# Optimization experiments

Measured on AMD Instinct MI355X. Metric: run time of the kernel, lower is better.

Reference implementation:

```python
import jax, jax.numpy as jnp
import numpy as np
from jax import lax

VOCAB, EMB, HID, B, T = 512, 128, 64, 256, 1024

def setup_inputs() -> dict:
    key = jax.random.key(0)
    ks = jax.random.split(key, 16)
    s = 0.1  # small init to keep tanh in its linear-ish range
    return {
        'x': jax.random.randint(ks[0], (B, T), 0, VOCAB),
        'emb': jax.random.normal(ks[1], (VOCAB, EMB), jnp.float32) * s,
        'Wih0': jax.random.normal(ks[2], (HID, EMB), jnp.float32) * s,
        'Whh0': jax.random.normal(ks[3], (HID, HID), jnp.float32) * s,
        'bih0': jax.random.normal(ks[4], (HID,), jnp.float32) * s,
        'bhh0': jax.random.normal(ks[5], (HID,), jnp.float32) * s,
        'Wih1': jax.random.normal(ks[6], (HID, HID), jnp.float32) * s,
        'Whh1': jax.random.normal(ks[7], (HID, HID), jnp.float32) * s,
        'bih1': jax.random.normal(ks[8], (HID,), jnp.float32) * s,
        'bhh1': jax.random.normal(ks[9], (HID,), jnp.float32) * s,
        'W1': jax.random.normal(ks[10], (32, HID), jnp.float32) * s,
        'b1': jax.random.normal(ks[11], (32,), jnp.float32) * s,
        'W2': jax.random.normal(ks[12], (1, 32), jnp.float32) * s,
        'b2': jax.random.normal(ks[13], (1,), jnp.float32) * s,
    }

def _rnn_layer(xs, Wih, Whh, bih, bhh):
    # xs: [T, B, D_in]; PyTorch cell: h_t = tanh(x W_ih^T + b_ih + h W_hh^T + b_hh)
    bsz = xs.shape[1]
    h0 = jnp.zeros((bsz, Whh.shape[0]), xs.dtype)
    def step(h, xt):
        h = jnp.tanh(xt @ Wih.T + bih + h @ Whh.T + bhh)
        return h, h
    hN, out = lax.scan(step, h0, xs)
    return hN, out

def reference(x, emb, Wih0, Whh0, bih0, bhh0, Wih1, Whh1, bih1, bhh1, W1, b1, W2, b2):
    xe = emb[x]                      # [B, T, EMB] embedding gather
    xs = jnp.swapaxes(xe, 0, 1)      # [T, B, EMB] time-major for scan
    _, out1 = _rnn_layer(xs, Wih0, Whh0, bih0, bhh0)   # layer 0 (dropout=0 in eval)
    hN, _ = _rnn_layer(out1, Wih1, Whh1, bih1, bhh1)   # layer 1; hN == h_n[-1]
    y = jnp.maximum(hN @ W1.T + b1, 0.0) @ W2.T + b2   # [B, 1]
    return y
```

## Files before the change

kernel.cpp:

```cpp
#include <hip/hip_runtime.h>

#define VOCAB 512
#define EMB   128
#define HID   64
#define BATCH 256
#define TLEN  1024
#define CH    8
#define NCH   (TLEN / CH)
#define RS    64
#define RCH   (RS / CH)
#define RW    80

typedef float v2f __attribute__((ext_vector_type(2)));

__device__ __forceinline__ float fast_tanh(float x) {
    float e = __expf(2.0f * x);
    return 1.0f - 2.0f / (e + 1.0f);
}
__device__ __forceinline__ void lds_fence() {
    asm volatile("s_waitcnt lgkmcnt(0)" ::: "memory");
}
__device__ __forceinline__ void compiler_fence() {
    asm volatile("" ::: "memory");
}
__device__ __forceinline__ void nap() { __builtin_amdgcn_s_sleep(1); }

__device__ __forceinline__ float quad_sum(float x) {
    int t1 = __builtin_amdgcn_update_dpp(0, __float_as_int(x), 0xB1, 0xF, 0xF, false);
    float s = x + __int_as_float(t1);
    int t2 = __builtin_amdgcn_update_dpp(0, __float_as_int(s), 0x4E, 0xF, 0xF, false);
    return s + __int_as_float(t2);
}

__device__ __forceinline__ float dot_seg(const float4 s[4], const v2f w[4][8],
                                         int kg) {
    float z0, z1, z2, z3;
    #pragma unroll
    for (int r = 0; r < 4; ++r) {
        v2f a0 = v2f{0.f, 0.f}, a1 = v2f{0.f, 0.f};
        #pragma unroll
        for (int c = 0; c < 4; ++c) {
            float4 u = s[c];
            a0 = __builtin_elementwise_fma(v2f{u.x, u.y}, w[r][2 * c],     a0);
            a1 = __builtin_elementwise_fma(v2f{u.z, u.w}, w[r][2 * c + 1], a1);
        }
        float zr = quad_sum((a0.x + a0.y) + (a1.x + a1.y));
        if (r == 0) z0 = zr; else if (r == 1) z1 = zr;
        else if (r == 2) z2 = zr; else z3 = zr;
    }
    return (kg & 1) ? ((kg & 2) ? z3 : z1) : ((kg & 2) ? z2 : z0);
}

__device__ __forceinline__ void load_w(v2f w[4][8], const float* __restrict__ W,
                                       int o, int kg) {
    #pragma unroll
    for (int r = 0; r < 4; ++r) {
        const float4* wr = (const float4*)(W + (o + 16 * r) * HID + 16 * kg);
        #pragma unroll
        for (int c = 0; c < 4; ++c) {
            float4 u = wr[c];
            w[r][2 * c]     = v2f{u.x, u.y};
            w[r][2 * c + 1] = v2f{u.z, u.w};
        }
    }
}

__device__ __forceinline__ void seg_load(float4 s[4], const float* rowkg) {
    const float4* p = (const float4*)rowkg;
    #pragma unroll
    for (int c = 0; c < 4; ++c) s[c] = p[c];
}

__global__ void __launch_bounds__(64) p0_kernel(
    const float* __restrict__ emb,
    const float* __restrict__ wih0,
    const float* __restrict__ bih0,
    const float* __restrict__ bhh0,
    float* __restrict__ P0)
{
    const int v = blockIdx.x;
    const int i = threadIdx.x;
    const float4* er = (const float4*)(emb  + v * EMB);
    const float4* wr = (const float4*)(wih0 + i * EMB);
    float a0 = 0.f, a1 = 0.f, a2 = 0.f, a3 = 0.f;
    #pragma unroll
    for (int k = 0; k < EMB / 4; ++k) {
        float4 e4 = er[k];
        float4 w4 = wr[k];
        a0 = fmaf(e4.x, w4.x, a0);
        a1 = fmaf(e4.y, w4.y, a1);
        a2 = fmaf(e4.z, w4.z, a2);
        a3 = fmaf(e4.w, w4.w, a3);
    }
    P0[v * HID + i] = (a0 + a1) + (a2 + a3) + bih0[i] + bhh0[i];
}

__global__ void __launch_bounds__(192, 1) rnn_kernel(
    const int*   __restrict__ xs,
    const float* __restrict__ P0,
    const float* __restrict__ Whh0,
    const float* __restrict__ Wih1,
    const float* __restrict__ Whh1,
    const float* __restrict__ bih1,
    const float* __restrict__ bhh1,
    const float* __restrict__ W1,
    const float* __restrict__ b1,
    const float* __restrict__ W2,
    const float* __restrict__ b2,
    float*       __restrict__ out)
{
    __shared__ float h0ring[RS][RW];
    __shared__ float p1ring[RS][HID];
    __shared__ float h1buf[2][RW];
    __shared__ int   flags[3];

    const int b    = blockIdx.x;
    const int tid  = threadIdx.x;
    const int wv   = tid >> 6;
    const int lane = tid & 63;
    const int o    = lane >> 2;
    const int kg   = lane & 3;
    const int row  = o + 16 * kg;
    const int wrs  = 20 * kg + o;

    const int* xrow = xs + b * TLEN;
    const int vz = (int)__builtin_amdgcn_mbcnt_lo(0u, 0u);

    if (tid < 3) flags[tid] = 0;
    __syncthreads();

    volatile int* vf = (volatile int*)flags;

    if (wv == 0) {
        v2f w0[4][8];
        load_w(w0, Whh0, o, kg);

        int   xv_old[CH];
        float a_old[CH];
        #pragma unroll
        for (int i = 0; i < CH; ++i)
            xv_old[i] = xrow[CH + i + vz] & (VOCAB - 1);
        #pragma unroll
        for (int i = 0; i < CH; ++i)
            a_old[i] = P0[(xrow[i + vz] & (VOCAB - 1)) * HID + row];

        float4 s0[4];
        #pragma unroll
        for (int c = 0; c < 4; ++c) s0[c] = float4{0.f, 0.f, 0.f, 0.f};

        #pragma unroll 1
        for (int k = 0; k < NCH; ++k) {
            if (k >= RCH) {
                while (vf[1] < k - (RCH - 1)) nap();
                compiler_fence();
            }
            const int  c2  = (k + 2 < NCH) ? (k + 2) : (NCH - 1);
            const int* xp  = xrow + c2 * CH;
            int   xv_new[CH];
            float a_new[CH];
            #pragma unroll
            for (int i = 0; i < CH; ++i)
                xv_new[i] = xp[i + vz] & (VOCAB - 1);
            #pragma unroll
            for (int i = 0; i < CH; ++i)
                a_new[i] = P0[xv_old[i] * HID + row];

            const int base = (k & (RCH - 1)) * CH;
            #pragma unroll
            for (int i = 0; i < CH; ++i) {
                float z  = dot_seg(s0, w0, kg) + a_old[i];
                float hv = fast_tanh(z);
                h0ring[base + i][wrs] = hv;
                seg_load(s0, &h0ring[base + i][20 * kg]);
            }
            lds_fence();
            if (lane == 0) vf[0] = k + 1;

            #pragma unroll
            for (int i = 0; i < CH; ++i) { a_old[i] = a_new[i]; xv_old[i] = xv_new[i]; }
        }
    } else if (wv == 1) {
        v2f wp[4][8];
        load_w(wp, Wih1, o, kg);
        const float b1s = bih1[row] + bhh1[row];

        #pragma unroll 1
        for (int k = 0; k < NCH; ++k) {
            while (vf[0] < k + 1) nap();
            if (k >= RCH) { while (vf[2] < k - (RCH - 1)) nap(); }
            compiler_fence();
            const int base = (k & (RCH - 1)) * CH;
            float4 c0[4];
            seg_load(c0, &h0ring[base][20 * kg]);
            #pragma unroll
            for (int i = 0; i < CH; ++i) {
                float4 nx[4];
                if (i < CH - 1) seg_load(nx, &h0ring[base + i + 1][20 * kg]);
                float pv = dot_seg(c0, wp, kg) + b1s;
                p1ring[base + i][row] = pv;
                if (i < CH - 1) {
                    #pragma unroll
                    for (int c = 0; c < 4; ++c) c0[c] = nx[c];
                }
            }
            lds_fence();
            if (lane == 0) vf[1] = k + 1;
        }
    } else {
        v2f w2[4][8];
        load_w(w2, Whh1, o, kg);

        float4 s1[4];
        #pragma unroll
        for (int c = 0; c < 4; ++c) s1[c] = float4{0.f, 0.f, 0.f, 0.f};

        #pragma unroll 1
        for (int k = 0; k < NCH; ++k) {
            while (vf[1] < k + 1) nap();
            compiler_fence();
            const int base = (k & (RCH - 1)) * CH;
            float p[CH];
            #pragma unroll
            for (int i = 0; i < CH; ++i) p[i] = p1ring[base + i][row];
            #pragma unroll
            for (int i = 0; i < CH; ++i) {
                const int t = k * CH + i;
                float z  = dot_seg(s1, w2, kg) + p[i];
                float hv = fast_tanh(z);
                h1buf[t & 1][wrs] = hv;
                seg_load(s1, &h1buf[t & 1][20 * kg]);
            }
            lds_fence();
            if (lane == 0) vf[2] = k + 1;
        }
        float r = 0.f;
        if (lane < 32) {
            float acc = b1[lane];
            const float* w1row = W1 + lane * HID;
            const float* hN    = h1buf[(TLEN - 1) & 1];
            #pragma unroll
            for (int j = 0; j < HID; ++j)
                acc = fmaf(w1row[j], hN[20 * (j >> 4) + (j & 15)], acc);
            r = fmaxf(acc, 0.f) * W2[lane];
        }
        #pragma unroll
        for (int off = 32; off > 0; off >>= 1) r += __shfl_down(r, off);
        if (lane == 0) out[b] = r + b2[0];
    }
}

extern "C" void kernel_launch(void* const* d_in, const int* in_sizes, int n_in,
                              void* d_out, int out_size, void* d_ws, size_t ws_size,
                              hipStream_t stream)
{
    const int*   x    = (const int*)d_in[0];
    const float* emb  = (const float*)d_in[1];
    const float* Wih0 = (const float*)d_in[2];
    const float* Whh0 = (const float*)d_in[3];
    const float* bih0 = (const float*)d_in[4];
    const float* bhh0 = (const float*)d_in[5];
    const float* Wih1 = (const float*)d_in[6];
    const float* Whh1 = (const float*)d_in[7];
    const float* bih1 = (const float*)d_in[8];
    const float* bhh1 = (const float*)d_in[9];
    const float* W1   = (const float*)d_in[10];
    const float* b1   = (const float*)d_in[11];
    const float* W2   = (const float*)d_in[12];
    const float* b2   = (const float*)d_in[13];

    float* P0 = (float*)d_ws;

    hipLaunchKernelGGL(p0_kernel, dim3(VOCAB), dim3(HID), 0, stream,
                       emb, Wih0, bih0, bhh0, P0);
    hipLaunchKernelGGL(rnn_kernel, dim3(BATCH), dim3(192), 0, stream,
                       x, P0, Whh0, Wih1, Whh1, bih1, bhh1,
                       W1, b1, W2, b2, (float*)d_out);
}
```

Baseline: 308.1 us.

## Process two batch rows per block to interleave independent recurrences

Each block now runs two batch sequences at once. Every wave interleaves the two independent recurrence chains (dot, tanh, LDS store and reload) so one chain's latency can hide behind the other's work. The grid is halved to 128 blocks, leaving half the CUs idle, and the LDS ring depth is halved so the doubled buffers still fit, which tightens the producer/consumer slack between waves.

```diff
diff --git a/kernel.cpp b/kernel.cpp
--- a/kernel.cpp
+++ b/kernel.cpp
@@ -7,7 +7,7 @@
 #define TLEN  1024
 #define CH    8
 #define NCH   (TLEN / CH)
-#define RS    64
+#define RS    32
 #define RCH   (RS / CH)
 #define RW    80
 
@@ -109,12 +109,13 @@
     const float* __restrict__ b2,
     float*       __restrict__ out)
 {
-    __shared__ float h0ring[RS][RW];
-    __shared__ float p1ring[RS][HID];
-    __shared__ float h1buf[2][RW];
+    __shared__ float h0ring[2][RS][RW];
+    __shared__ float p1ring[2][RS][HID];
+    __shared__ float h1buf[2][2][RW];
     __shared__ int   flags[3];
 
-    const int b    = blockIdx.x;
+    const int b0   = blockIdx.x * 2;
+    const int b1i  = b0 + 1;
     const int tid  = threadIdx.x;
     const int wv   = tid >> 6;
     const int lane = tid & 63;
@@ -123,7 +124,8 @@
     const int row  = o + 16 * kg;
     const int wrs  = 20 * kg + o;
 
-    const int* xrow = xs + b * TLEN;
+    const int* xr0 = xs + b0  * TLEN;
+    const int* xr1 = xs + b1i * TLEN;
     const int vz = (int)__builtin_amdgcn_mbcnt_lo(0u, 0u);
 
     if (tid < 3) flags[tid] = 0;
@@ -135,18 +137,25 @@
         v2f w0[4][8];
         load_w(w0, Whh0, o, kg);
 
-        int   xv_old[CH];
-        float a_old[CH];
-        #pragma unroll
-        for (int i = 0; i < CH; ++i)
-            xv_old[i] = xrow[CH + i + vz] & (VOCAB - 1);
-        #pragma unroll
-        for (int i = 0; i < CH; ++i)
-            a_old[i] = P0[(xrow[i + vz] & (VOCAB - 1)) * HID + row];
-
-        float4 s0[4];
-        #pragma unroll
-        for (int c = 0; c < 4; ++c) s0[c] = float4{0.f, 0.f, 0.f, 0.f};
+        int   xv_old[2][CH];
+        float a_old[2][CH];
+        #pragma unroll
+        for (int i = 0; i < CH; ++i) {
+            xv_old[0][i] = xr0[CH + i + vz] & (VOCAB - 1);
+            xv_old[1][i] = xr1[CH + i + vz] & (VOCAB - 1);
+        }
+        #pragma unroll
+        for (int i = 0; i < CH; ++i) {
+            a_old[0][i] = P0[(xr0[i + vz] & (VOCAB - 1)) * HID + row];
+            a_old[1][i] = P0[(xr1[i + vz] & (VOCAB - 1)) * HID + row];
+        }
+
+        float4 s0[4], s1[4];
+        #pragma unroll
+        for (int c = 0; c < 4; ++c) {
+            s0[c] = float4{0.f, 0.f, 0.f, 0.f};
+            s1[c] = float4{0.f, 0.f, 0.f, 0.f};
+        }
 
         #pragma unroll 1
         for (int k = 0; k < NCH; ++k) {
@@ -155,29 +164,41 @@
                 compiler_fence();
             }
             const int  c2  = (k + 2 < NCH) ? (k + 2) : (NCH - 1);
-            const int* xp  = xrow + c2 * CH;
-            int   xv_new[CH];
-            float a_new[CH];
-            #pragma unroll
-            for (int i = 0; i < CH; ++i)
-                xv_new[i] = xp[i + vz] & (VOCAB - 1);
-            #pragma unroll
-            for (int i = 0; i < CH; ++i)
-                a_new[i] = P0[xv_old[i] * HID + row];
+            const int* xp0 = xr0 + c2 * CH;
+            const int* xp1 = xr1 + c2 * CH;
+            int   xv_new[2][CH];
+            float a_new[2][CH];
+            #pragma unroll
+            for (int i = 0; i < CH; ++i) {
+                xv_new[0][i] = xp0[i + vz] & (VOCAB - 1);
+                xv_new[1][i] = xp1[i + vz] & (VOCAB - 1);
+            }
+            #pragma unroll
+            for (int i = 0; i < CH; ++i) {
+                a_new[0][i] = P0[xv_old[0][i] * HID + row];
+                a_new[1][i] = P0[xv_old[1][i] * HID + row];
+            }
 
             const int base = (k & (RCH - 1)) * CH;
             #pragma unroll
             for (int i = 0; i < CH; ++i) {
-                float z  = dot_seg(s0, w0, kg) + a_old[i];
-                float hv = fast_tanh(z);
-                h0ring[base + i][wrs] = hv;
-                seg_load(s0, &h0ring[base + i][20 * kg]);
+                float z0  = dot_seg(s0, w0, kg) + a_old[0][i];
+                float z1  = dot_seg(s1, w0, kg) + a_old[1][i];
+                float h0v = fast_tanh(z0);
+                float h1v = fast_tanh(z1);
+                h0ring[0][base + i][wrs] = h0v;
+                h0ring[1][base + i][wrs] = h1v;
+                seg_load(s0, &h0ring[0][base + i][20 * kg]);
+                seg_load(s1, &h0ring[1][base + i][20 * kg]);
             }
             lds_fence();
             if (lane == 0) vf[0] = k + 1;
 
             #pragma unroll
-            for (int i = 0; i < CH; ++i) { a_old[i] = a_new[i]; xv_old[i] = xv_new[i]; }
+            for (int i = 0; i < CH; ++i) {
+                a_old[0][i] = a_new[0][i]; xv_old[0][i] = xv_new[0][i];
+                a_old[1][i] = a_new[1][i]; xv_old[1][i] = xv_new[1][i];
+            }
         }
     } else if (wv == 1) {
         v2f wp[4][8];
@@ -190,17 +211,23 @@
             if (k >= RCH) { while (vf[2] < k - (RCH - 1)) nap(); }
             compiler_fence();
             const int base = (k & (RCH - 1)) * CH;
-            float4 c0[4];
-            seg_load(c0, &h0ring[base][20 * kg]);
-            #pragma unroll
-            for (int i = 0; i < CH; ++i) {
-                float4 nx[4];
-                if (i < CH - 1) seg_load(nx, &h0ring[base + i + 1][20 * kg]);
-                float pv = dot_seg(c0, wp, kg) + b1s;
-                p1ring[base + i][row] = pv;
+            float4 c0[4], c1[4];
+            seg_load(c0, &h0ring[0][base][20 * kg]);
+            seg_load(c1, &h0ring[1][base][20 * kg]);
+            #pragma unroll
+            for (int i = 0; i < CH; ++i) {
+                float4 n0[4], n1[4];
+                if (i < CH - 1) {
+                    seg_load(n0, &h0ring[0][base + i + 1][20 * kg]);
+                    seg_load(n1, &h0ring[1][base + i + 1][20 * kg]);
+                }
+                float pv0 = dot_seg(c0, wp, kg) + b1s;
+                float pv1 = dot_seg(c1, wp, kg) + b1s;
+                p1ring[0][base + i][row] = pv0;
+                p1ring[1][base + i][row] = pv1;
                 if (i < CH - 1) {
                     #pragma unroll
-                    for (int c = 0; c < 4; ++c) c0[c] = nx[c];
+                    for (int c = 0; c < 4; ++c) { c0[c] = n0[c]; c1[c] = n1[c]; }
                 }
             }
             lds_fence();
@@ -210,42 +237,55 @@
         v2f w2[4][8];
         load_w(w2, Whh1, o, kg);
 
-        float4 s1[4];
-        #pragma unroll
-        for (int c = 0; c < 4; ++c) s1[c] = float4{0.f, 0.f, 0.f, 0.f};
+        float4 s0[4], s1[4];
+        #pragma unroll
+        for (int c = 0; c < 4; ++c) {
+            s0[c] = float4{0.f, 0.f, 0.f, 0.f};
+            s1[c] = float4{0.f, 0.f, 0.f, 0.f};
+        }
 
         #pragma unroll 1
         for (int k = 0; k < NCH; ++k) {
             while (vf[1] < k + 1) nap();
             compiler_fence();
             const int base = (k & (RCH - 1)) * CH;
-            float p[CH];
-            #pragma unroll
-            for (int i = 0; i < CH; ++i) p[i] = p1ring[base + i][row];
+            float p0v[CH], p1v[CH];
+            #pragma unroll
+            for (int i = 0; i < CH; ++i) {
+                p0v[i] = p1ring[0][base + i][row];
+                p1v[i] = p1ring[1][base + i][row];
+            }
             #pragma unroll
             for (int i = 0; i < CH; ++i) {
                 const int t = k * CH + i;
-                float z  = dot_seg(s1, w2, kg) + p[i];
-                float hv = fast_tanh(z);
-                h1buf[t & 1][wrs] = hv;
-                seg_load(s1, &h1buf[t & 1][20 * kg]);
+                float z0  = dot_seg(s0, w2, kg) + p0v[i];
+                float z1  = dot_seg(s1, w2, kg) + p1v[i];
+                float h0v = fast_tanh(z0);
+                float h1v = fast_tanh(z1);
+                h1buf[0][t & 1][wrs] = h0v;
+                h1buf[1][t & 1][wrs] = h1v;
+                seg_load(s0, &h1buf[0][t & 1][20 * kg]);
+                seg_load(s1, &h1buf[1][t & 1][20 * kg]);
             }
             lds_fence();
             if (lane == 0) vf[2] = k + 1;
         }
-        float r = 0.f;
-        if (lane < 32) {
-            float acc = b1[lane];
-            const float* w1row = W1 + lane * HID;
-            const float* hN    = h1buf[(TLEN - 1) & 1];
-            #pragma unroll
-            for (int j = 0; j < HID; ++j)
-                acc = fmaf(w1row[j], hN[20 * (j >> 4) + (j & 15)], acc);
-            r = fmaxf(acc, 0.f) * W2[lane];
-        }
-        #pragma unroll
-        for (int off = 32; off > 0; off >>= 1) r += __shfl_down(r, off);
-        if (lane == 0) out[b] = r + b2[0];
+        #pragma unroll 1
+        for (int s = 0; s < 2; ++s) {
+            float r = 0.f;
+            if (lane < 32) {
+                float acc = b1[lane];
+                const float* w1row = W1 + lane * HID;
+                const float* hN    = h1buf[s][(TLEN - 1) & 1];
+                #pragma unroll
+                for (int j = 0; j < HID; ++j)
+                    acc = fmaf(w1row[j], hN[20 * (j >> 4) + (j & 15)], acc);
+                r = fmaxf(acc, 0.f) * W2[lane];
+            }
+            #pragma unroll
+            for (int off = 32; off > 0; off >>= 1) r += __shfl_down(r, off);
+            if (lane == 0) out[b0 + s] = r + b2[0];
+        }
     }
 }
 
@@ -272,7 +312,7 @@
 
     hipLaunchKernelGGL(p0_kernel, dim3(VOCAB), dim3(HID), 0, stream,
                        emb, Wih0, bih0, bhh0, P0);
-    hipLaunchKernelGGL(rnn_kernel, dim3(BATCH), dim3(192), 0, stream,
+    hipLaunchKernelGGL(rnn_kernel, dim3(BATCH / 2), dim3(192), 0, stream,
                        x, P0, Whh0, Wih1, Whh1, bih1, bhh1,
                        W1, b1, W2, b2, (float*)d_out);
 }
```

New measurement: 472.1 us. 1.53x slower.

## Add producer wavefront to prefetch embedding projections into LDS ring

Applied to the files above, without the earlier changes.

Adds a fourth wavefront that reads token indices and gathers the precomputed P0 rows from global memory into an LDS ring, signalling the layer-0 recurrence wave through a new flag. The layer-0 wave no longer issues global loads or keeps software-prefetch registers; it reads its inputs from LDS. This is meant to take global-memory latency off the serial critical path. In exchange it adds LDS traffic, another flag handshake per chunk, and a fourth wave per block.

```diff
diff --git a/kernel.cpp b/kernel.cpp
--- a/kernel.cpp
+++ b/kernel.cpp
@@ -95,7 +95,7 @@
     P0[v * HID + i] = (a0 + a1) + (a2 + a3) + bih0[i] + bhh0[i];
 }
 
-__global__ void __launch_bounds__(192, 1) rnn_kernel(
+__global__ void __launch_bounds__(256, 1) rnn_kernel(
     const int*   __restrict__ xs,
     const float* __restrict__ P0,
     const float* __restrict__ Whh0,
@@ -109,10 +109,11 @@
     const float* __restrict__ b2,
     float*       __restrict__ out)
 {
+    __shared__ float a_ring[RS][HID];
     __shared__ float h0ring[RS][RW];
     __shared__ float p1ring[RS][HID];
     __shared__ float h1buf[2][RW];
-    __shared__ int   flags[3];
+    __shared__ int   flags[4];
 
     const int b    = blockIdx.x;
     const int tid  = threadIdx.x;
@@ -126,7 +127,7 @@
     const int* xrow = xs + b * TLEN;
     const int vz = (int)__builtin_amdgcn_mbcnt_lo(0u, 0u);
 
-    if (tid < 3) flags[tid] = 0;
+    if (tid < 4) flags[tid] = 0;
     __syncthreads();
 
     volatile int* vf = (volatile int*)flags;
@@ -135,49 +136,30 @@
         v2f w0[4][8];
         load_w(w0, Whh0, o, kg);
 
-        int   xv_old[CH];
-        float a_old[CH];
-        #pragma unroll
-        for (int i = 0; i < CH; ++i)
-            xv_old[i] = xrow[CH + i + vz] & (VOCAB - 1);
-        #pragma unroll
-        for (int i = 0; i < CH; ++i)
-            a_old[i] = P0[(xrow[i + vz] & (VOCAB - 1)) * HID + row];
-
         float4 s0[4];
         #pragma unroll
         for (int c = 0; c < 4; ++c) s0[c] = float4{0.f, 0.f, 0.f, 0.f};
 
         #pragma unroll 1
         for (int k = 0; k < NCH; ++k) {
+            while (vf[3] < k + 1) nap();
             if (k >= RCH) {
                 while (vf[1] < k - (RCH - 1)) nap();
-                compiler_fence();
-            }
-            const int  c2  = (k + 2 < NCH) ? (k + 2) : (NCH - 1);
-            const int* xp  = xrow + c2 * CH;
-            int   xv_new[CH];
-            float a_new[CH];
-            #pragma unroll
-            for (int i = 0; i < CH; ++i)
-                xv_new[i] = xp[i + vz] & (VOCAB - 1);
-            #pragma unroll
-            for (int i = 0; i < CH; ++i)
-                a_new[i] = P0[xv_old[i] * HID + row];
-
-            const int base = (k & (RCH - 1)) * CH;
+            }
+            compiler_fence();
+            const int base = (k & (RCH - 1)) * CH;
+            float a8[CH];
+            #pragma unroll
+            for (int i = 0; i < CH; ++i) a8[i] = a_ring[base + i][row];
             #pragma unroll
             for (int i = 0; i < CH; ++i) {
-                float z  = dot_seg(s0, w0, kg) + a_old[i];
+                float z  = dot_seg(s0, w0, kg) + a8[i];
                 float hv = fast_tanh(z);
                 h0ring[base + i][wrs] = hv;
                 seg_load(s0, &h0ring[base + i][20 * kg]);
             }
             lds_fence();
             if (lane == 0) vf[0] = k + 1;
-
-            #pragma unroll
-            for (int i = 0; i < CH; ++i) { a_old[i] = a_new[i]; xv_old[i] = xv_new[i]; }
         }
     } else if (wv == 1) {
         v2f wp[4][8];
@@ -206,7 +188,7 @@
             lds_fence();
             if (lane == 0) vf[1] = k + 1;
         }
-    } else {
+    } else if (wv == 2) {
         v2f w2[4][8];
         load_w(w2, Whh1, o, kg);
 
@@ -246,6 +228,29 @@
         #pragma unroll
         for (int off = 32; off > 0; off >>= 1) r += __shfl_down(r, off);
         if (lane == 0) out[b] = r + b2[0];
+    } else {
+        #pragma unroll 1
+        for (int k = 0; k < NCH; ++k) {
+            if (k >= RCH) {
+                while (vf[0] < k - (RCH - 1)) nap();
+                compiler_fence();
+            }
+            const int* xp = xrow + k * CH;
+            int xv[CH];
+            #pragma unroll
+            for (int i = 0; i < CH; ++i)
+                xv[i] = xp[i + vz] & (VOCAB - 1);
+            float av[CH];
+            #pragma unroll
+            for (int i = 0; i < CH; ++i)
+                av[i] = P0[xv[i] * HID + row];
+            const int base = (k & (RCH - 1)) * CH;
+            #pragma unroll
+            for (int i = 0; i < CH; ++i)
+                a_ring[base + i][row] = av[i];
+            lds_fence();
+            if (lane == 0) vf[3] = k + 1;
+        }
     }
 }
 
@@ -272,7 +277,7 @@
 
     hipLaunchKernelGGL(p0_kernel, dim3(VOCAB), dim3(HID), 0, stream,
                        emb, Wih0, bih0, bhh0, P0);
-    hipLaunchKernelGGL(rnn_kernel, dim3(BATCH), dim3(192), 0, stream,
+    hipLaunchKernelGGL(rnn_kernel, dim3(BATCH), dim3(256), 0, stream,
                        x, P0, Whh0, Wih1, Whh1, bih1, bhh1,
                        W1, b1, W2, b2, (float*)d_out);
 }
```

Result: faster. 299.3 us (-2.9%).
